# Kernel tuning notes

Hardware: AMD Instinct MI355X
Metric: run time of the kernel (lower is better)

Reference implementation:

```python
import jax, jax.numpy as jnp
import numpy as np

CHUNK_LEN = 32
N_HEAD = 32
HEAD_SIZE = 64
EPS = 1e-5 * 64.0  # GroupNorm eps = 1e-5 * head_size_divisor**2
PREC_MIN = 0.005   # rwkv_inner precision_min_val clamp for fp32


def rwkv_inner(r, k, v, w, u, kv_state, chunk_len):
    # r,k,v,w: [B,H,L,K]; u: [H,K]; kv_state: [B,H,K,V]
    B, H, L, K = k.shape
    T = chunk_len
    N = L // T
    w = jnp.clip(w, PREC_MIN, None)
    wc_log = jnp.log(w).reshape(B, H, N, T, K)
    wc_cum = jnp.cumsum(wc_log, axis=-2)                      # [B,H,N,T,K]
    shifted = jnp.concatenate([jnp.zeros_like(wc_cum[..., :1, :]), wc_cum[..., :-1, :]], axis=-2)
    ws_log = jnp.sum(wc_log, axis=-2, keepdims=True)          # [B,H,N,1,K]
    w_inter = jnp.exp(ws_log - wc_cum)                        # decay to end of chunk
    w_intra = jnp.exp(wc_cum - wc_log)                        # decay from start of chunk
    rc = r.reshape(B, H, N, T, K)
    kc = k.reshape(B, H, N, T, K)
    vc = v.reshape(B, H, N, T, K)
    # intra-chunk attention, log-space offset at T//2 for numerical stability
    off = shifted[..., T // 2:T // 2 + 1, :]
    r_decay = jnp.exp(shifted - off)
    k_inv_decay = jnp.exp(off - wc_cum)
    a = jnp.einsum('bhntk,bhnsk->bhnts', rc * r_decay, kc * k_inv_decay)
    a = jnp.tril(a, -1)
    diag = jnp.einsum('bhntk,bhntk->bhnt', rc, u[None, :, None, None, :] * kc)
    out = jnp.einsum('bhnts,bhnsv->bhntv', a, vc) + diag[..., None] * vc
    # per-chunk (k*w_inter)^T @ v contributions, then sequential state carry
    wkv = jnp.einsum('bhntk,bhntv->bhnkv', kc * w_inter, vc)  # [B,H,N,K,V]
    ws = jnp.exp(ws_log)[:, :, :, 0, :]                       # [B,H,N,K]

    def step(state, xs):
        ws_i, wkv_i = xs
        new_state = state * ws_i[..., None] + wkv_i
        return new_state, state

    final_state, states = jax.lax.scan(step, kv_state, (jnp.moveaxis(ws, 2, 0), jnp.moveaxis(wkv, 2, 0)))
    states = jnp.moveaxis(states, 0, 2)                       # [B,H,N,K,V]
    out = out + jnp.einsum('bhntk,bhnkv->bhntv', rc * w_intra, states)
    return out.reshape(B, H, L, K), final_state


def _forward(x, shift_state, wkv_state,
             time_maa_x, time_maa_w, time_maa_k, time_maa_v, time_maa_r, time_maa_g,
             time_maa_w1, time_maa_w2, time_decay, time_decay_w1, time_decay_w2,
             time_faaaa, Wr, Wk, Wv, Wg, Wo, gn_w, gn_b):
    B, T, C = x.shape
    H, K = N_HEAD, HEAD_SIZE
    xprev = jnp.concatenate([shift_state[:, None, :], x[:, :-1]], axis=1)
    dx = xprev - x
    # token-shift LoRA mixing
    xxx = jnp.tanh((x + dx * time_maa_x) @ time_maa_w1).reshape(B, T, 5, -1)
    m = jnp.einsum('btfe,fec->fbtc', xxx, time_maa_w2)  # [5,B,T,C]
    mw, mk, mv, mr, mg = m[0], m[1], m[2], m[3], m[4]
    xk = x + dx * (time_maa_k + mk)
    xv = x + dx * (time_maa_v + mv)
    xr = x + dx * (time_maa_r + mr)
    xg = x + dx * (time_maa_g + mg)
    xw = x + dx * (time_maa_w + mw)
    r = (xr @ Wr.T).reshape(B, T, H, K).transpose(0, 2, 1, 3)
    k = (xk @ Wk.T).reshape(B, T, H, K).transpose(0, 2, 1, 3)
    v = (xv @ Wv.T).reshape(B, T, H, K).transpose(0, 2, 1, 3)
    g = jax.nn.silu(xg @ Wg.T)
    w = time_decay.reshape(1, H, 1, K) + (jnp.tanh(xw @ time_decay_w1) @ time_decay_w2).reshape(B, T, H, K).transpose(0, 2, 1, 3)
    w = jnp.exp(-jnp.exp(w))
    out, wkv_out = rwkv_inner(r, k, v, w, time_faaaa, wkv_state, CHUNK_LEN)
    out = out.transpose(0, 2, 1, 3).reshape(B, T, C)
    # GroupNorm with H groups of K channels
    og = out.reshape(B, T, H, K)
    mu = og.mean(-1, keepdims=True)
    var = og.var(-1, keepdims=True)
    og = (og - mu) * jax.lax.rsqrt(var + EPS)
    out = og.reshape(B, T, C) * gn_w + gn_b
    out = (out * g) @ Wo.T
    return out, x[:, -1], wkv_out


def setup_inputs() -> dict:
    B, T, C = 4, 2048, 2048
    H, K = N_HEAD, HEAD_SIZE
    E5, TD = 32, 64
    key = jax.random.key(0)
    ks = jax.random.split(key, 24)
    f32 = jnp.float32
    inp = {
        'x': jax.random.normal(ks[0], (B, T, C), f32),
        'shift_state': jax.random.normal(ks[1], (B, C), f32),
        'wkv_state': jax.random.normal(ks[2], (B, H, K, K), f32) * 0.1,
        'time_maa_x': jax.random.uniform(ks[3], (1, 1, C), f32),
        'time_maa_w': jax.random.uniform(ks[4], (1, 1, C), f32),
        'time_maa_k': jax.random.uniform(ks[5], (1, 1, C), f32),
        'time_maa_v': jax.random.uniform(ks[6], (1, 1, C), f32),
        'time_maa_r': jax.random.uniform(ks[7], (1, 1, C), f32),
        'time_maa_g': jax.random.uniform(ks[8], (1, 1, C), f32),
        'time_maa_w1': jax.random.uniform(ks[9], (C, E5 * 5), f32, -1e-4, 1e-4),
        'time_maa_w2': jax.random.normal(ks[10], (5, E5, C), f32) * 0.01,
        'time_decay': jnp.linspace(-6.0, -1.0, C, dtype=f32).reshape(1, 1, C),
        'time_decay_w1': jax.random.uniform(ks[11], (C, TD), f32, -1e-4, 1e-4),
        'time_decay_w2': jax.random.normal(ks[12], (TD, C), f32) * 0.01,
        'time_faaaa': jax.random.normal(ks[13], (H, K), f32) * 0.1,
        'Wr': jax.random.normal(ks[14], (C, C), f32) * 0.02,
        'Wk': jax.random.normal(ks[15], (C, C), f32) * 0.02,
        'Wv': jax.random.normal(ks[16], (C, C), f32) * 0.02,
        'Wg': jax.random.normal(ks[17], (C, C), f32) * 0.02,
        'Wo': jax.random.normal(ks[18], (C, C), f32) * 0.02,
        'gn_w': jnp.ones((C,), f32),
        'gn_b': jnp.zeros((C,), f32),
    }
    return inp


def reference(x, shift_state, wkv_state,
              time_maa_x, time_maa_w, time_maa_k, time_maa_v, time_maa_r, time_maa_g,
              time_maa_w1, time_maa_w2, time_decay, time_decay_w1, time_decay_w2,
              time_faaaa, Wr, Wk, Wv, Wg, Wo, gn_w, gn_b):
    return _forward(x, shift_state, wkv_state,
                    time_maa_x, time_maa_w, time_maa_k, time_maa_v, time_maa_r, time_maa_g,
                    time_maa_w1, time_maa_w2, time_decay, time_decay_w1, time_decay_w2,
                    time_faaaa, Wr, Wk, Wv, Wg, Wo, gn_w, gn_b)
```

## Files before the change

### kernel.cpp

```cpp
#include <hip/hip_runtime.h>
#include <stdint.h>
#include <math.h>


typedef __attribute__((ext_vector_type(8))) short bf16x8;
typedef __attribute__((ext_vector_type(4))) float f32x4;

#define AS1(p) ((const __attribute__((address_space(1))) void*)(p))
#define AS3(p) ((__attribute__((address_space(3))) void*)(p))

__device__ __forceinline__ unsigned short f2bf(float f) {
  unsigned int u = __builtin_bit_cast(unsigned int, f);
  u += 0x7fffu + ((u >> 16) & 1u);
  return (unsigned short)(u >> 16);
}
__device__ __forceinline__ float bf2f(unsigned short s) {
  unsigned int u = ((unsigned int)s) << 16;
  return __builtin_bit_cast(float, u);
}

template <int EPI, bool BOUNDS>
__global__ __launch_bounds__(256) void gemm_nt(
    const unsigned short* __restrict__ A, const unsigned short* __restrict__ B,
    void* __restrict__ Cp, int M, int N, int K, const float* __restrict__ evec,
    int slot)
{
  __shared__ __align__(16) unsigned short As[128 * 32];
  __shared__ __align__(16) unsigned short Bs[128 * 32];
  const int tid = threadIdx.x;
  const int l = tid & 63, w = tid >> 6;
  const int wm = w & 1, wn = w >> 1;
  const int lm = l & 15, quad = l >> 4;
  const long mBase = (long)blockIdx.y * 128;
  const long nBase = (long)blockIdx.x * 128;

  f32x4 acc[4][4];
  f32x4 zero = {0.f, 0.f, 0.f, 0.f};
#pragma unroll
  for (int i = 0; i < 4; i++)
#pragma unroll
    for (int j = 0; j < 4; j++) acc[i][j] = zero;

  for (int k0 = 0; k0 < K; k0 += 32) {
    if (!BOUNDS) {
      const int r0 = w * 32;
      const int lr = l >> 2, lc = l & 3;
      const unsigned short* gA = A + (mBase + r0 + lr) * (long)K + k0 + lc * 8;
      __builtin_amdgcn_global_load_lds(AS1(gA), AS3(&As[r0 * 32]), 16, 0, 0);
      const unsigned short* gA2 = gA + 16 * (long)K;
      __builtin_amdgcn_global_load_lds(AS1(gA2), AS3(&As[(r0 + 16) * 32]), 16, 0, 0);
      const unsigned short* gB = B + (nBase + r0 + lr) * (long)K + k0 + lc * 8;
      __builtin_amdgcn_global_load_lds(AS1(gB), AS3(&Bs[r0 * 32]), 16, 0, 0);
      const unsigned short* gB2 = gB + 16 * (long)K;
      __builtin_amdgcn_global_load_lds(AS1(gB2), AS3(&Bs[(r0 + 16) * 32]), 16, 0, 0);
    } else {
      const int row = tid >> 2, ch = tid & 3;
#pragma unroll
      for (int rr = 0; rr < 128; rr += 64) {
        int r = rr + row;
        *(int4*)&As[r * 32 + ch * 8] =
            *(const int4*)&A[(mBase + r) * (long)K + k0 + ch * 8];
        int4 bv = make_int4(0, 0, 0, 0);
        long nG = nBase + r;
        if (nG < N) bv = *(const int4*)&B[nG * (long)K + k0 + ch * 8];
        *(int4*)&Bs[r * 32 + ch * 8] = bv;
      }
    }
    __syncthreads();
    bf16x8 af[4], bq[4];
#pragma unroll
    for (int i = 0; i < 4; i++)
      af[i] = *(const bf16x8*)&As[(wm * 64 + i * 16 + lm) * 32 + quad * 8];
#pragma unroll
    for (int i = 0; i < 4; i++)
      bq[i] = *(const bf16x8*)&Bs[(wn * 64 + i * 16 + lm) * 32 + quad * 8];
#pragma unroll
    for (int mi = 0; mi < 4; mi++)
#pragma unroll
      for (int ni = 0; ni < 4; ni++)
        acc[mi][ni] = __builtin_amdgcn_mfma_f32_16x16x32_bf16(af[mi], bq[ni], acc[mi][ni], 0, 0, 0);
    __syncthreads();
  }

#pragma unroll
  for (int mi = 0; mi < 4; mi++) {
#pragma unroll
    for (int ni = 0; ni < 4; ni++) {
      long col = nBase + wn * 64 + ni * 16 + lm;
      if (BOUNDS && col >= N) continue;
      long rw0 = mBase + wm * 64 + mi * 16 + quad * 4;
#pragma unroll
      for (int r = 0; r < 4; r++) {
        float y = acc[mi][ni][r];
        long row = rw0 + r;
        long off = row * (long)N + col;
        if constexpr (EPI == 0) {
          ((float*)Cp)[off] = y;
        } else if constexpr (EPI == 2) {
          ((unsigned short*)Cp)[off] = f2bf(tanhf(y));
        } else if constexpr (EPI == 3) {
          ((unsigned short*)Cp)[off] = f2bf(y / (1.f + __expf(-y)));
        } else if constexpr (EPI == 4) {
          float wv = evec[col] + y;
          ((_Float16*)Cp)[off] = (_Float16)fmaxf(-__expf(wv), -5.2983174f);
        } else if constexpr (EPI == 5) {
          int b = (int)(row >> 11), t = (int)(row & 2047);
          int n = t >> 5, tt = t & 31;
          int h = (int)(col >> 6), kk = (int)(col & 63);
          long c = ((long)(b * 32 + h)) * 64 + n;
          ((unsigned short*)Cp)[c * 6144 + slot + tt * 64 + kk] = f2bf(y);
        }
      }
    }
  }
}

template <int EPI>
__global__ __launch_bounds__(512, 1) void gemm256_nt(
    const unsigned short* __restrict__ A, const unsigned short* __restrict__ B,
    void* __restrict__ Cp, int M, int N, int K, int slot)
{
  __shared__ __align__(16) unsigned short As2[2][16384];
  __shared__ __align__(16) unsigned short Bs2[2][16384];
  const int tid = threadIdx.x;
  const int l = tid & 63;
  const int w = tid >> 6;
  const int wm = w >> 2, wn = w & 3;
  const int lm = l & 15, quad = l >> 4;
  const long mBase = (long)blockIdx.y * 256;
  const long nBase = (long)blockIdx.x * 256;
  const int NT = K >> 6;

  const int r0 = tid >> 3;
  const int csw = (tid & 7) ^ (r0 & 7);
  const int ldsOff = (tid & ~63) * 8;
  const unsigned short* ga0 = A + (mBase + r0) * (long)K + csw * 8;
  const unsigned short* gb0 = B + (nBase + r0) * (long)K + csw * 8;

  f32x4 acc[8][4];
  f32x4 zero = {0.f, 0.f, 0.f, 0.f};
#pragma unroll
  for (int i = 0; i < 8; i++)
#pragma unroll
    for (int j = 0; j < 4; j++) acc[i][j] = zero;

#define STAGE256(kt_)                                                          \
  {                                                                            \
    const int _b = (kt_) & 1;                                                  \
    const unsigned short* _ga = ga0 + (long)(kt_) * 64;                        \
    const unsigned short* _gb = gb0 + (long)(kt_) * 64;                        \
    __builtin_amdgcn_global_load_lds(AS1(_ga), AS3(&As2[_b][ldsOff]), 16, 0, 0);              \
    __builtin_amdgcn_global_load_lds(AS1(_gb), AS3(&Bs2[_b][ldsOff]), 16, 0, 0);              \
    __builtin_amdgcn_global_load_lds(AS1(_ga + (long)64 * K), AS3(&As2[_b][4096 + ldsOff]), 16, 0, 0);  \
    __builtin_amdgcn_global_load_lds(AS1(_gb + (long)64 * K), AS3(&Bs2[_b][4096 + ldsOff]), 16, 0, 0);  \
    __builtin_amdgcn_global_load_lds(AS1(_ga + (long)128 * K), AS3(&As2[_b][8192 + ldsOff]), 16, 0, 0); \
    __builtin_amdgcn_global_load_lds(AS1(_gb + (long)128 * K), AS3(&Bs2[_b][8192 + ldsOff]), 16, 0, 0); \
    __builtin_amdgcn_global_load_lds(AS1(_ga + (long)192 * K), AS3(&As2[_b][12288 + ldsOff]), 16, 0, 0);\
    __builtin_amdgcn_global_load_lds(AS1(_gb + (long)192 * K), AS3(&Bs2[_b][12288 + ldsOff]), 16, 0, 0);\
  }

  STAGE256(0);
  STAGE256(1);
  asm volatile("s_waitcnt vmcnt(8)" ::: "memory");
  __builtin_amdgcn_s_barrier();

  const int q0 = (quad ^ (lm & 7)) * 8;
  const int rA = (wm * 128 + lm) * 64;
  const int rB = (wn * 64 + lm) * 64;

  for (int kt = 0; kt < NT; ++kt) {
    const int b = kt & 1;
    bf16x8 af[8][2], bq[4][2];
#pragma unroll
    for (int fm = 0; fm < 8; fm++)
      af[fm][0] = *(const bf16x8*)&As2[b][rA + fm * 1024 + q0];
#pragma unroll
    for (int fn = 0; fn < 4; fn++)
      bq[fn][0] = *(const bf16x8*)&Bs2[b][rB + fn * 1024 + q0];
#pragma unroll
    for (int fm = 0; fm < 8; fm++)
      af[fm][1] = *(const bf16x8*)&As2[b][rA + fm * 1024 + (q0 ^ 32)];
#pragma unroll
    for (int fn = 0; fn < 4; fn++)
      bq[fn][1] = *(const bf16x8*)&Bs2[b][rB + fn * 1024 + (q0 ^ 32)];

    __builtin_amdgcn_s_setprio(1);
#pragma unroll
    for (int fm = 0; fm < 8; fm++)
#pragma unroll
      for (int fn = 0; fn < 4; fn++)
        acc[fm][fn] = __builtin_amdgcn_mfma_f32_16x16x32_bf16(af[fm][0], bq[fn][0], acc[fm][fn], 0, 0, 0);
    __builtin_amdgcn_s_setprio(0);

    asm volatile("s_waitcnt lgkmcnt(0)" ::: "memory");
    __builtin_amdgcn_s_barrier();
    if (kt + 2 < NT) STAGE256(kt + 2);

    __builtin_amdgcn_s_setprio(1);
#pragma unroll
    for (int fm = 0; fm < 8; fm++)
#pragma unroll
      for (int fn = 0; fn < 4; fn++)
        acc[fm][fn] = __builtin_amdgcn_mfma_f32_16x16x32_bf16(af[fm][1], bq[fn][1], acc[fm][fn], 0, 0, 0);
    __builtin_amdgcn_s_setprio(0);

    if (kt + 2 < NT) {
      asm volatile("s_waitcnt vmcnt(8)" ::: "memory");
    } else {
      asm volatile("s_waitcnt vmcnt(0)" ::: "memory");
    }
    __builtin_amdgcn_s_barrier();
  }
#undef STAGE256

#pragma unroll
  for (int mi = 0; mi < 8; mi++) {
#pragma unroll
    for (int ni = 0; ni < 4; ni++) {
      long col = nBase + wn * 64 + ni * 16 + lm;
      long rw0 = mBase + wm * 128 + mi * 16 + quad * 4;
#pragma unroll
      for (int r = 0; r < 4; r++) {
        float y = acc[mi][ni][r];
        long row = rw0 + r;
        long off = row * (long)N + col;
        if constexpr (EPI == 0) {
          ((float*)Cp)[off] = y;
        } else if constexpr (EPI == 3) {
          ((unsigned short*)Cp)[off] = f2bf(y / (1.f + __expf(-y)));
        } else if constexpr (EPI == 5) {
          int bb = (int)(row >> 11), t = (int)(row & 2047);
          int n = t >> 5, tt = t & 31;
          int h = (int)(col >> 6), kk = (int)(col & 63);
          long c = ((long)(bb * 32 + h)) * 64 + n;
          ((unsigned short*)Cp)[c * 6144 + slot + tt * 64 + kk] = f2bf(y);
        }
      }
    }
  }
}

__global__ __launch_bounds__(256) void k_convert(const float* __restrict__ s,
                                                 unsigned short* __restrict__ d, int n4)
{
  int i = blockIdx.x * 256 + threadIdx.x;
  if (i >= n4) return;
  float4 v = ((const float4*)s)[i];
  short4 o;
  o.x = (short)f2bf(v.x); o.y = (short)f2bf(v.y);
  o.z = (short)f2bf(v.z); o.w = (short)f2bf(v.w);
  ((short4*)d)[i] = o;
}

__global__ __launch_bounds__(256) void k_transpose(const float* __restrict__ s,
                                                   unsigned short* __restrict__ d, int R, int C)
{
  int i = blockIdx.x * 256 + threadIdx.x;
  if (i >= R * C) return;
  int r = i / C, c = i - r * C;
  d[(long)c * R + r] = f2bf(s[i]);
}

__global__ __launch_bounds__(256) void k_prep(const float* __restrict__ x,
                                              const float* __restrict__ shift,
                                              const float* __restrict__ maax,
                                              unsigned short* __restrict__ xmix,
                                              float* __restrict__ xlast)
{
  int i = blockIdx.x * 256 + threadIdx.x;
  int c4 = (i & 511) * 4;
  long bt = i >> 9;
  int t = (int)(bt & 2047);
  long b = bt >> 11;
  float4 xv = *(const float4*)&x[bt * 2048 + c4];
  float4 xp;
  if (t == 0) xp = *(const float4*)&shift[b * 2048 + c4];
  else        xp = *(const float4*)&x[(bt - 1) * 2048 + c4];
  float4 mx = *(const float4*)&maax[c4];
  short4 o;
  o.x = (short)f2bf(xv.x + (xp.x - xv.x) * mx.x);
  o.y = (short)f2bf(xv.y + (xp.y - xv.y) * mx.y);
  o.z = (short)f2bf(xv.z + (xp.z - xv.z) * mx.z);
  o.w = (short)f2bf(xv.w + (xp.w - xv.w) * mx.w);
  *(short4*)&xmix[bt * 2048 + c4] = o;
  if (t == 2047) *(float4*)&xlast[b * 2048 + c4] = xv;
}

__global__ __launch_bounds__(256) void k_mix1(
    const unsigned short* __restrict__ xxx, const unsigned short* __restrict__ w2t,
    const float* __restrict__ x, const float* __restrict__ shift,
    const float* __restrict__ maa, unsigned short* __restrict__ xout, int f)
{
  __shared__ __align__(16) unsigned short As[128 * 32];
  __shared__ __align__(16) unsigned short Bs[128 * 32];
  const int tid = threadIdx.x;
  const int l = tid & 63, w = tid >> 6;
  const int wm = w & 1, wn = w >> 1;
  const int lm = l & 15, quad = l >> 4;
  const long mBase = (long)blockIdx.y * 128;
  const long nBase = (long)blockIdx.x * 128;
  const int row = tid >> 2, ch = tid & 3;
#pragma unroll
  for (int rr = 0; rr < 128; rr += 64) {
    int r = rr + row;
    *(int4*)&As[r * 32 + ch * 8] =
        *(const int4*)&xxx[(mBase + r) * 160 + f * 32 + ch * 8];
    *(int4*)&Bs[r * 32 + ch * 8] =
        *(const int4*)&w2t[((long)f * 2048 + nBase + r) * 32 + ch * 8];
  }
  __syncthreads();
  f32x4 zero = {0.f, 0.f, 0.f, 0.f};
  f32x4 acc[4][4];
#pragma unroll
  for (int i = 0; i < 4; i++)
#pragma unroll
    for (int j = 0; j < 4; j++) acc[i][j] = zero;
  bf16x8 af[4], bq[4];
#pragma unroll
  for (int i = 0; i < 4; i++)
    af[i] = *(const bf16x8*)&As[(wm * 64 + i * 16 + lm) * 32 + quad * 8];
#pragma unroll
  for (int i = 0; i < 4; i++)
    bq[i] = *(const bf16x8*)&Bs[(wn * 64 + i * 16 + lm) * 32 + quad * 8];
#pragma unroll
  for (int mi = 0; mi < 4; mi++)
#pragma unroll
    for (int ni = 0; ni < 4; ni++)
      acc[mi][ni] = __builtin_amdgcn_mfma_f32_16x16x32_bf16(af[mi], bq[ni], acc[mi][ni], 0, 0, 0);

#pragma unroll
  for (int mi = 0; mi < 4; mi++) {
#pragma unroll
    for (int ni = 0; ni < 4; ni++) {
      long col = nBase + wn * 64 + ni * 16 + lm;
#pragma unroll
      for (int r = 0; r < 4; r++) {
        long rg = mBase + wm * 64 + mi * 16 + quad * 4 + r;
        int t = (int)(rg & 2047);
        long b = rg >> 11;
        float xval = x[rg * 2048 + col];
        float xp = t ? x[(rg - 1) * 2048 + col] : shift[b * 2048 + col];
        float res = xval + (xp - xval) * (maa[col] + acc[mi][ni][r]);
        xout[rg * 2048 + col] = f2bf(res);
      }
    }
  }
}

__global__ __launch_bounds__(256) void k_chunk(
    unsigned short* __restrict__ recs, const _Float16* __restrict__ wl,
    const float* __restrict__ u, float* __restrict__ outw,
    float* __restrict__ wsb)
{
  const int chunk = blockIdx.x;
  const int n = chunk & 63, bh = chunk >> 6;
  const int h = bh & 31, b = bh >> 5;
  const int tid = threadIdx.x;
  const int lane = tid & 63, wvid = tid >> 6;
  const long rec = (long)chunk * 6144;
  const long tbase = ((long)(b * 2048 + n * 32)) * 2048 + h * 64;

  __shared__ float vc[32][65];
  __shared__ float wcum[32][65];
  __shared__ float rdec[32][65];
  __shared__ float kdec[32][65];
  __shared__ float amat[32][33];
  __shared__ float wsk[64];

  float rcr[8], kcr[8];
#pragma unroll
  for (int j = 0; j < 8; j++) {
    int t = wvid + 4 * j;
    long g = rec + t * 64 + lane;
    rcr[j] = bf2f(recs[g]);
    kcr[j] = bf2f(recs[g + 2048]);
    vc[t][lane] = bf2f(recs[g + 4096]);
    wcum[t][lane] = (float)wl[tbase + (long)t * 2048 + lane];
  }
  float uval = u[h * 64 + lane];
  __syncthreads();

  if (tid < 64) {
    float run = 0.f;
    for (int t = 0; t < 32; t++) { run += wcum[t][tid]; wcum[t][tid] = run; }
    wsk[tid] = run;
  }
  __syncthreads();

  const float offv = wcum[15][lane];
  const float wsv = wsk[lane];
  float rdr[8], kdr[8], klr[8], rwir[8], dpart[8];
#pragma unroll
  for (int j = 0; j < 8; j++) {
    int t = wvid + 4 * j;
    float cw = wcum[t][lane];
    float sh = t ? wcum[t - 1][lane] : 0.f;
    rwir[j] = rcr[j] * __expf(sh);
    rdr[j] = rcr[j] * __expf(sh - offv);
    kdr[j] = kcr[j] * __expf(offv - cw);
    klr[j] = kcr[j] * __expf(wsv - cw);
    dpart[j] = rcr[j] * uval * kcr[j];
  }
  __syncthreads();

#pragma unroll
  for (int j = 0; j < 8; j++) {
    int t = wvid + 4 * j;
    rdec[t][lane] = rdr[j];
    kdec[t][lane] = kdr[j];
    wcum[t][lane] = klr[j];
    recs[rec + 4096 + t * 64 + lane] = f2bf(rwir[j]);
  }
  if (tid < 64) wsb[(long)chunk * 64 + tid] = __expf(wsk[tid]);
  __syncthreads();

  {
    const int t0 = (tid >> 4) * 2, s0 = (tid & 15) * 2;
    float a00 = 0, a01 = 0, a10 = 0, a11 = 0;
    for (int kk = 0; kk < 64; kk++) {
      float r0 = rdec[t0][kk], r1 = rdec[t0 + 1][kk];
      float c0 = kdec[s0][kk], c1 = kdec[s0 + 1][kk];
      a00 += r0 * c0; a01 += r0 * c1; a10 += r1 * c0; a11 += r1 * c1;
    }
    amat[t0][s0]         = (s0     < t0)     ? a00 : 0.f;
    amat[t0][s0 + 1]     = (s0 + 1 < t0)     ? a01 : 0.f;
    amat[t0 + 1][s0]     = (s0     < t0 + 1) ? a10 : 0.f;
    amat[t0 + 1][s0 + 1] = (s0 + 1 < t0 + 1) ? a11 : 0.f;
  }
  __syncthreads();
#pragma unroll
  for (int j = 0; j < 8; j++) {
    float d = dpart[j];
#pragma unroll
    for (int m = 32; m; m >>= 1) d += __shfl_xor(d, m, 64);
    if (lane == 0) amat[wvid + 4 * j][wvid + 4 * j] = d;
  }
  __syncthreads();

  {
    const int t0 = (tid >> 4) * 2, v0 = (tid & 15) * 4;
    float o00 = 0, o01 = 0, o02 = 0, o03 = 0, o10 = 0, o11 = 0, o12 = 0, o13 = 0;
    for (int s = 0; s < 32; s++) {
      float a0 = amat[t0][s], a1 = amat[t0 + 1][s];
      float b0 = vc[s][v0], b1 = vc[s][v0 + 1], b2 = vc[s][v0 + 2], b3 = vc[s][v0 + 3];
      o00 += a0 * b0; o01 += a0 * b1; o02 += a0 * b2; o03 += a0 * b3;
      o10 += a1 * b0; o11 += a1 * b1; o12 += a1 * b2; o13 += a1 * b3;
    }
    float* p0 = &outw[tbase + (long)t0 * 2048 + v0];
    float* p1 = &outw[tbase + (long)(t0 + 1) * 2048 + v0];
    p0[0] = o00; p0[1] = o01; p0[2] = o02; p0[3] = o03;
    p1[0] = o10; p1[1] = o11; p1[2] = o12; p1[3] = o13;
  }

  {
    const int kk0 = (tid >> 4) * 4, v0 = (tid & 15) * 4;
    float a[4][4];
#pragma unroll
    for (int i = 0; i < 4; i++)
#pragma unroll
      for (int j = 0; j < 4; j++) a[i][j] = 0.f;
    for (int t = 0; t < 32; t++) {
      float w0 = wcum[t][kk0], w1 = wcum[t][kk0 + 1], w2 = wcum[t][kk0 + 2], w3 = wcum[t][kk0 + 3];
      float b0 = vc[t][v0], b1 = vc[t][v0 + 1], b2 = vc[t][v0 + 2], b3 = vc[t][v0 + 3];
      a[0][0] += w0 * b0; a[0][1] += w0 * b1; a[0][2] += w0 * b2; a[0][3] += w0 * b3;
      a[1][0] += w1 * b0; a[1][1] += w1 * b1; a[1][2] += w1 * b2; a[1][3] += w1 * b3;
      a[2][0] += w2 * b0; a[2][1] += w2 * b1; a[2][2] += w2 * b2; a[2][3] += w2 * b3;
      a[3][0] += w3 * b0; a[3][1] += w3 * b1; a[3][2] += w3 * b2; a[3][3] += w3 * b3;
    }
#pragma unroll
    for (int i = 0; i < 4; i++)
#pragma unroll
      for (int j = 0; j < 4; j++)
        recs[rec + (kk0 + i) * 64 + v0 + j] = f2bf(a[i][j]);
  }
}

__global__ __launch_bounds__(256) void k_scan(unsigned short* __restrict__ recs,
                                              const float* __restrict__ wsb,
                                              const float* __restrict__ kv0,
                                              float* __restrict__ finalst)
{
  const int bh = blockIdx.x >> 2;
  const int kq = blockIdx.x & 3;
  const int tid = threadIdx.x;
  float st[4];
  const long base = (long)bh * 4096 + kq * 1024;
#pragma unroll
  for (int j = 0; j < 4; j++) st[j] = kv0[base + j * 256 + tid];
  for (int n = 0; n < 64; n++) {
    const long cb = ((long)bh * 64 + n) * 6144 + kq * 1024;
    const long wb = ((long)bh * 64 + n) * 64 + kq * 16;
#pragma unroll
    for (int j = 0; j < 4; j++) {
      int i = j * 256 + tid;
      unsigned short* p = &recs[cb + i];
      float wv = bf2f(*p);
      *p = f2bf(st[j]);
      st[j] = st[j] * wsb[wb + (i >> 6)] + wv;
    }
  }
#pragma unroll
  for (int j = 0; j < 4; j++) finalst[base + j * 256 + tid] = st[j];
}

__global__ __launch_bounds__(256) void k_inter(const unsigned short* __restrict__ recs,
                                               float* __restrict__ outw)
{
  const int chunk = blockIdx.x;
  const int n = chunk & 63, bh = chunk >> 6;
  const int h = bh & 31, b = bh >> 5;
  const int tid = threadIdx.x;
  __shared__ float st[64][65];
  __shared__ float rw[32][65];
  const long rec = (long)chunk * 6144;
  for (int i = tid; i < 4096; i += 256) st[i >> 6][i & 63] = bf2f(recs[rec + i]);
  for (int i = tid; i < 2048; i += 256) rw[i >> 6][i & 63] = bf2f(recs[rec + 4096 + i]);
  __syncthreads();
  const long tbase = ((long)(b * 2048 + n * 32)) * 2048 + h * 64;
  const int t0 = (tid >> 4) * 2, v0 = (tid & 15) * 4;
  float o00 = 0, o01 = 0, o02 = 0, o03 = 0, o10 = 0, o11 = 0, o12 = 0, o13 = 0;
  for (int kk = 0; kk < 64; kk++) {
    float r0 = rw[t0][kk], r1 = rw[t0 + 1][kk];
    float s0 = st[kk][v0], s1 = st[kk][v0 + 1], s2 = st[kk][v0 + 2], s3 = st[kk][v0 + 3];
    o00 += r0 * s0; o01 += r0 * s1; o02 += r0 * s2; o03 += r0 * s3;
    o10 += r1 * s0; o11 += r1 * s1; o12 += r1 * s2; o13 += r1 * s3;
  }
  float* p0 = &outw[tbase + (long)t0 * 2048 + v0];
  float* p1 = &outw[tbase + (long)(t0 + 1) * 2048 + v0];
  p0[0] += o00; p0[1] += o01; p0[2] += o02; p0[3] += o03;
  p1[0] += o10; p1[1] += o11; p1[2] += o12; p1[3] += o13;
}

__global__ __launch_bounds__(256) void k_gnorm(const float* __restrict__ outw,
                                               const unsigned short* __restrict__ gb,
                                               const float* __restrict__ gnw,
                                               const float* __restrict__ gnb,
                                               unsigned short* __restrict__ aout)
{
  const int gid = blockIdx.x * 4 + (threadIdx.x >> 6);
  const int lane = threadIdx.x & 63;
  const long bt = gid >> 5;
  const int h = gid & 31;
  const int c = h * 64 + lane;
  const long off = bt * 2048 + c;
  float y = outw[off];
  float s = y, sq = y * y;
#pragma unroll
  for (int m = 32; m; m >>= 1) {
    s += __shfl_xor(s, m, 64);
    sq += __shfl_xor(sq, m, 64);
  }
  float mu = s * (1.f / 64.f);
  float var = sq * (1.f / 64.f) - mu * mu;
  float nrm = (y - mu) * rsqrtf(var + 6.4e-4f);
  float o = (nrm * gnw[c] + gnb[c]) * bf2f(gb[off]);
  aout[off] = f2bf(o);
}

extern "C" void kernel_launch(void* const* d_in, const int* in_sizes, int n_in,
                              void* d_out, int out_size, void* d_ws, size_t ws_size,
                              hipStream_t stream)
{
  const float* x     = (const float*)d_in[0];
  const float* shift = (const float*)d_in[1];
  const float* kv0   = (const float*)d_in[2];
  const float* maax  = (const float*)d_in[3];
  const float* maaw  = (const float*)d_in[4];
  const float* maak  = (const float*)d_in[5];
  const float* maav  = (const float*)d_in[6];
  const float* maar  = (const float*)d_in[7];
  const float* maag  = (const float*)d_in[8];
  const float* w1    = (const float*)d_in[9];
  const float* w2    = (const float*)d_in[10];
  const float* tdec  = (const float*)d_in[11];
  const float* tdw1  = (const float*)d_in[12];
  const float* tdw2  = (const float*)d_in[13];
  const float* u     = (const float*)d_in[14];
  const float* Wr    = (const float*)d_in[15];
  const float* Wk    = (const float*)d_in[16];
  const float* Wv    = (const float*)d_in[17];
  const float* Wg    = (const float*)d_in[18];
  const float* Wo    = (const float*)d_in[19];
  const float* gnw   = (const float*)d_in[20];
  const float* gnb   = (const float*)d_in[21];

  char* ws = (char*)d_ws;
  const size_t MB = 1048576;
  unsigned short* WbfR  = (unsigned short*)(ws + 0 * MB);
  unsigned short* WbfK  = (unsigned short*)(ws + 8 * MB);
  unsigned short* WbfV  = (unsigned short*)(ws + 16 * MB);
  unsigned short* WbfG  = (unsigned short*)(ws + 24 * MB);
  unsigned short* WbfO  = (unsigned short*)(ws + 32 * MB);
  unsigned short* w2tb  = (unsigned short*)(ws + 40 * MB);
  unsigned short* w1t   = (unsigned short*)(ws + 40 * MB + 655360);
  unsigned short* tdw1t = (unsigned short*)(ws + 40 * MB + 1310720);
  unsigned short* tdw2t = (unsigned short*)(ws + 40 * MB + 1572864);
  unsigned short* xxxb  = (unsigned short*)(ws + 40 * MB + 1835008);
  unsigned short* t1b   = (unsigned short*)(ws + 40 * MB + 4456448);
  float*          wsb   = (float*)(ws + 40 * MB + 5505024);
  unsigned short* xmixb = (unsigned short*)(ws + 48 * MB);
  _Float16*       wlb   = (_Float16*)(ws + 48 * MB);
  unsigned short* x1b   = (unsigned short*)(ws + 80 * MB);
  unsigned short* aob   = (unsigned short*)(ws + 80 * MB);
  unsigned short* recs  = (unsigned short*)(ws + 112 * MB);
  unsigned short* gbuf  = recs;

  float* outp    = (float*)d_out;
  float* xlast   = outp + 16777216;
  float* finalst = outp + 16777216 + 8192;

  k_convert<<<4096, 256, 0, stream>>>(Wr, WbfR, 1048576);
  k_convert<<<4096, 256, 0, stream>>>(Wk, WbfK, 1048576);
  k_convert<<<4096, 256, 0, stream>>>(Wv, WbfV, 1048576);
  k_convert<<<4096, 256, 0, stream>>>(Wg, WbfG, 1048576);
  k_convert<<<4096, 256, 0, stream>>>(Wo, WbfO, 1048576);
  k_transpose<<<1280, 256, 0, stream>>>(w1, w1t, 2048, 160);
  k_transpose<<<512, 256, 0, stream>>>(tdw1, tdw1t, 2048, 64);
  k_transpose<<<512, 256, 0, stream>>>(tdw2, tdw2t, 64, 2048);
  for (int f = 0; f < 5; f++)
    k_transpose<<<256, 256, 0, stream>>>(w2 + (long)f * 65536, w2tb + (long)f * 65536, 32, 2048);

  k_prep<<<16384, 256, 0, stream>>>(x, shift, maax, xmixb, xlast);
  gemm_nt<2, true><<<dim3(2, 64), 256, 0, stream>>>(xmixb, w1t, xxxb, 8192, 160, 2048, nullptr, 0);

  k_mix1<<<dim3(16, 64), 256, 0, stream>>>(xxxb, w2tb, x, shift, maaw, x1b, 0);
  gemm_nt<2, true><<<dim3(1, 64), 256, 0, stream>>>(x1b, tdw1t, t1b, 8192, 64, 2048, nullptr, 0);
  gemm_nt<4, false><<<dim3(16, 64), 256, 0, stream>>>(t1b, tdw2t, wlb, 8192, 2048, 64, tdec, 0);
  k_mix1<<<dim3(16, 64), 256, 0, stream>>>(xxxb, w2tb, x, shift, maak, x1b, 1);
  gemm256_nt<5><<<dim3(8, 32), 512, 0, stream>>>(x1b, WbfK, recs, 8192, 2048, 2048, 2048);
  k_mix1<<<dim3(16, 64), 256, 0, stream>>>(xxxb, w2tb, x, shift, maav, x1b, 2);
  gemm256_nt<5><<<dim3(8, 32), 512, 0, stream>>>(x1b, WbfV, recs, 8192, 2048, 2048, 4096);
  k_mix1<<<dim3(16, 64), 256, 0, stream>>>(xxxb, w2tb, x, shift, maar, x1b, 3);
  gemm256_nt<5><<<dim3(8, 32), 512, 0, stream>>>(x1b, WbfR, recs, 8192, 2048, 2048, 0);
  k_mix1<<<dim3(16, 64), 256, 0, stream>>>(xxxb, w2tb, x, shift, maag, x1b, 4);

  k_chunk<<<8192, 256, 0, stream>>>(recs, wlb, u, outp, wsb);
  k_scan<<<512, 256, 0, stream>>>(recs, wsb, kv0, finalst);
  k_inter<<<8192, 256, 0, stream>>>(recs, outp);

  gemm256_nt<3><<<dim3(8, 32), 512, 0, stream>>>(x1b, WbfG, gbuf, 8192, 2048, 2048, 0);
  k_gnorm<<<65536, 256, 0, stream>>>(outp, gbuf, gnw, gnb, aob);
  gemm256_nt<0><<<dim3(8, 32), 512, 0, stream>>>(aob, WbfO, outp, 8192, 2048, 2048, 0);
}
```

Baseline: 1.281 ms.

## Use bf16 MFMA with hi/lo split in chunk and inter-chunk kernels

Replaces scalar FP32 shared-memory matmuls in k_chunk (A·V and k_decay^T·V) and k_inter (r·state) with 16x16x32 bf16 MFMA instructions. Values are staged transposed in shared memory, and the attention matrix and decayed keys are split into hi/lo bf16 pairs to keep close to fp32 accuracy. The per-chunk cumulative-sum is also parallelised across waves using partial sums instead of a single 64-thread serial loop. The chunk and inter kernels are a small share of the total runtime, which is likely dominated by the large GEMMs. The extra split MFMAs and transposed stores cost some work in exchange.

```diff
diff --git a/kernel.cpp b/kernel.cpp
--- a/kernel.cpp
+++ b/kernel.cpp
@@ -17,6 +17,9 @@
 __device__ __forceinline__ float bf2f(unsigned short s) {
   unsigned int u = ((unsigned int)s) << 16;
   return __builtin_bit_cast(float, u);
+}
+__device__ __forceinline__ unsigned int packbf(float lo, float hi) {
+  return (unsigned int)f2bf(lo) | ((unsigned int)f2bf(hi) << 16);
 }
 
 template <int EPI, bool BOUNDS>
@@ -356,122 +359,157 @@
   const int n = chunk & 63, bh = chunk >> 6;
   const int h = bh & 31, b = bh >> 5;
   const int tid = threadIdx.x;
-  const int lane = tid & 63, wvid = tid >> 6;
+  const int lane = tid & 63, w = tid >> 6;
+  const int lm = lane & 15, quad = lane >> 4;
   const long rec = (long)chunk * 6144;
   const long tbase = ((long)(b * 2048 + n * 32)) * 2048 + h * 64;
 
-  __shared__ float vc[32][65];
-  __shared__ float wcum[32][65];
-  __shared__ float rdec[32][65];
-  __shared__ float kdec[32][65];
-  __shared__ float amat[32][33];
-  __shared__ float wsk[64];
-
-  float rcr[8], kcr[8];
+  __shared__ float rdec[32][68];
+  __shared__ float kdec[32][68];
+  __shared__ float ssum[4][64];
+  __shared__ float offr[64];
+  __shared__ float diagr[32];
+  __shared__ __align__(16) unsigned short amatH[32][40];
+  __shared__ __align__(16) unsigned short amatL[32][40];
+  __shared__ __align__(16) unsigned short vcT[64][40];
+  __shared__ __align__(16) unsigned short kwH[64][40];
+  __shared__ __align__(16) unsigned short kwL[64][40];
+
+  float rv[8], kv[8], wlog[8], cum[8];
 #pragma unroll
   for (int j = 0; j < 8; j++) {
-    int t = wvid + 4 * j;
+    int t = w * 8 + j;
     long g = rec + t * 64 + lane;
-    rcr[j] = bf2f(recs[g]);
-    kcr[j] = bf2f(recs[g + 2048]);
-    vc[t][lane] = bf2f(recs[g + 4096]);
-    wcum[t][lane] = (float)wl[tbase + (long)t * 2048 + lane];
-  }
-  float uval = u[h * 64 + lane];
+    rv[j] = bf2f(recs[g]);
+    kv[j] = bf2f(recs[g + 2048]);
+    wlog[j] = (float)wl[tbase + (long)t * 2048 + lane];
+  }
+  {
+    float run = 0.f;
+#pragma unroll
+    for (int j = 0; j < 8; j++) { run += wlog[j]; cum[j] = run; }
+    ssum[w][lane] = run;
+  }
+#pragma unroll
+  for (int jp = 0; jp < 4; jp++) {
+    int t0 = w * 8 + jp * 2;
+    float v0 = bf2f(recs[rec + (t0) * 64 + lane + 4096]);
+    float v1 = bf2f(recs[rec + (t0 + 1) * 64 + lane + 4096]);
+    *(unsigned int*)&vcT[lane][t0] = packbf(v0, v1);
+  }
   __syncthreads();
 
-  if (tid < 64) {
-    float run = 0.f;
-    for (int t = 0; t < 32; t++) { run += wcum[t][tid]; wcum[t][tid] = run; }
-    wsk[tid] = run;
-  }
+  float off = 0.f, tot = 0.f;
+#pragma unroll
+  for (int w2 = 0; w2 < 4; w2++) {
+    float s2 = ssum[w2][lane];
+    tot += s2;
+    if (w2 < w) off += s2;
+  }
+#pragma unroll
+  for (int j = 0; j < 8; j++) cum[j] += off;
+  if (w == 1) offr[lane] = cum[7];
+  if (w == 0) wsb[(long)chunk * 64 + lane] = __expf(tot);
   __syncthreads();
 
-  const float offv = wcum[15][lane];
-  const float wsv = wsk[lane];
-  float rdr[8], kdr[8], klr[8], rwir[8], dpart[8];
+  const float offv = offr[lane];
+  const float uval = u[h * 64 + lane];
+#pragma unroll
+  for (int jp = 0; jp < 4; jp++) {
+    unsigned short h2[2], l2[2];
+#pragma unroll
+    for (int p = 0; p < 2; p++) {
+      int j = jp * 2 + p;
+      int t = w * 8 + j;
+      float cw = cum[j];
+      float sh = cw - wlog[j];
+      rdec[t][lane] = rv[j] * __expf(sh - offv);
+      kdec[t][lane] = kv[j] * __expf(offv - cw);
+      float kw_ = kv[j] * __expf(tot - cw);
+      h2[p] = f2bf(kw_);
+      l2[p] = f2bf(kw_ - bf2f(h2[p]));
+      recs[rec + 4096 + t * 64 + lane] = f2bf(rv[j] * __expf(sh));
+    }
+    *(unsigned int*)&kwH[lane][w * 8 + jp * 2] = (unsigned int)h2[0] | ((unsigned int)h2[1] << 16);
+    *(unsigned int*)&kwL[lane][w * 8 + jp * 2] = (unsigned int)l2[0] | ((unsigned int)l2[1] << 16);
+  }
 #pragma unroll
   for (int j = 0; j < 8; j++) {
-    int t = wvid + 4 * j;
-    float cw = wcum[t][lane];
-    float sh = t ? wcum[t - 1][lane] : 0.f;
-    rwir[j] = rcr[j] * __expf(sh);
-    rdr[j] = rcr[j] * __expf(sh - offv);
-    kdr[j] = kcr[j] * __expf(offv - cw);
-    klr[j] = kcr[j] * __expf(wsv - cw);
-    dpart[j] = rcr[j] * uval * kcr[j];
+    float d = rv[j] * uval * kv[j];
+#pragma unroll
+    for (int m = 32; m; m >>= 1) d += __shfl_xor(d, m, 64);
+    if (lane == 0) diagr[w * 8 + j] = d;
   }
   __syncthreads();
 
-#pragma unroll
-  for (int j = 0; j < 8; j++) {
-    int t = wvid + 4 * j;
-    rdec[t][lane] = rdr[j];
-    kdec[t][lane] = kdr[j];
-    wcum[t][lane] = klr[j];
-    recs[rec + 4096 + t * 64 + lane] = f2bf(rwir[j]);
-  }
-  if (tid < 64) wsb[(long)chunk * 64 + tid] = __expf(wsk[tid]);
+  {
+    const int t0 = (tid >> 4) * 2;
+    const int sA = tid & 15;
+    float a00 = 0, a01 = 0, a10 = 0, a11 = 0;
+#pragma unroll
+    for (int kk = 0; kk < 64; kk += 4) {
+      float4 r0 = *(const float4*)&rdec[t0][kk];
+      float4 r1 = *(const float4*)&rdec[t0 + 1][kk];
+      float4 c0 = *(const float4*)&kdec[sA][kk];
+      float4 c1 = *(const float4*)&kdec[sA + 16][kk];
+      a00 += r0.x * c0.x + r0.y * c0.y + r0.z * c0.z + r0.w * c0.w;
+      a01 += r0.x * c1.x + r0.y * c1.y + r0.z * c1.z + r0.w * c1.w;
+      a10 += r1.x * c0.x + r1.y * c0.y + r1.z * c0.z + r1.w * c0.w;
+      a11 += r1.x * c1.x + r1.y * c1.y + r1.z * c1.z + r1.w * c1.w;
+    }
+    const int sB = sA + 16;
+    float m00 = sA < t0 ? a00 : (sA == t0 ? diagr[t0] : 0.f);
+    float m01 = sB < t0 ? a01 : (sB == t0 ? diagr[t0] : 0.f);
+    float m10 = sA < t0 + 1 ? a10 : (sA == t0 + 1 ? diagr[t0 + 1] : 0.f);
+    float m11 = sB < t0 + 1 ? a11 : (sB == t0 + 1 ? diagr[t0 + 1] : 0.f);
+    unsigned short h00 = f2bf(m00), h01 = f2bf(m01), h10 = f2bf(m10), h11 = f2bf(m11);
+    amatH[t0][sA] = h00;     amatL[t0][sA] = f2bf(m00 - bf2f(h00));
+    amatH[t0][sB] = h01;     amatL[t0][sB] = f2bf(m01 - bf2f(h01));
+    amatH[t0 + 1][sA] = h10; amatL[t0 + 1][sA] = f2bf(m10 - bf2f(h10));
+    amatH[t0 + 1][sB] = h11; amatL[t0 + 1][sB] = f2bf(m11 - bf2f(h11));
+  }
   __syncthreads();
 
   {
-    const int t0 = (tid >> 4) * 2, s0 = (tid & 15) * 2;
-    float a00 = 0, a01 = 0, a10 = 0, a11 = 0;
-    for (int kk = 0; kk < 64; kk++) {
-      float r0 = rdec[t0][kk], r1 = rdec[t0 + 1][kk];
-      float c0 = kdec[s0][kk], c1 = kdec[s0 + 1][kk];
-      a00 += r0 * c0; a01 += r0 * c1; a10 += r1 * c0; a11 += r1 * c1;
-    }
-    amat[t0][s0]         = (s0     < t0)     ? a00 : 0.f;
-    amat[t0][s0 + 1]     = (s0 + 1 < t0)     ? a01 : 0.f;
-    amat[t0 + 1][s0]     = (s0     < t0 + 1) ? a10 : 0.f;
-    amat[t0 + 1][s0 + 1] = (s0 + 1 < t0 + 1) ? a11 : 0.f;
-  }
-  __syncthreads();
-#pragma unroll
-  for (int j = 0; j < 8; j++) {
-    float d = dpart[j];
-#pragma unroll
-    for (int m = 32; m; m >>= 1) d += __shfl_xor(d, m, 64);
-    if (lane == 0) amat[wvid + 4 * j][wvid + 4 * j] = d;
-  }
-  __syncthreads();
-
-  {
-    const int t0 = (tid >> 4) * 2, v0 = (tid & 15) * 4;
-    float o00 = 0, o01 = 0, o02 = 0, o03 = 0, o10 = 0, o11 = 0, o12 = 0, o13 = 0;
-    for (int s = 0; s < 32; s++) {
-      float a0 = amat[t0][s], a1 = amat[t0 + 1][s];
-      float b0 = vc[s][v0], b1 = vc[s][v0 + 1], b2 = vc[s][v0 + 2], b3 = vc[s][v0 + 3];
-      o00 += a0 * b0; o01 += a0 * b1; o02 += a0 * b2; o03 += a0 * b3;
-      o10 += a1 * b0; o11 += a1 * b1; o12 += a1 * b2; o13 += a1 * b3;
-    }
-    float* p0 = &outw[tbase + (long)t0 * 2048 + v0];
-    float* p1 = &outw[tbase + (long)(t0 + 1) * 2048 + v0];
-    p0[0] = o00; p0[1] = o01; p0[2] = o02; p0[3] = o03;
-    p1[0] = o10; p1[1] = o11; p1[2] = o12; p1[3] = o13;
-  }
-
-  {
-    const int kk0 = (tid >> 4) * 4, v0 = (tid & 15) * 4;
-    float a[4][4];
-#pragma unroll
-    for (int i = 0; i < 4; i++)
-#pragma unroll
-      for (int j = 0; j < 4; j++) a[i][j] = 0.f;
-    for (int t = 0; t < 32; t++) {
-      float w0 = wcum[t][kk0], w1 = wcum[t][kk0 + 1], w2 = wcum[t][kk0 + 2], w3 = wcum[t][kk0 + 3];
-      float b0 = vc[t][v0], b1 = vc[t][v0 + 1], b2 = vc[t][v0 + 2], b3 = vc[t][v0 + 3];
-      a[0][0] += w0 * b0; a[0][1] += w0 * b1; a[0][2] += w0 * b2; a[0][3] += w0 * b3;
-      a[1][0] += w1 * b0; a[1][1] += w1 * b1; a[1][2] += w1 * b2; a[1][3] += w1 * b3;
-      a[2][0] += w2 * b0; a[2][1] += w2 * b1; a[2][2] += w2 * b2; a[2][3] += w2 * b3;
-      a[3][0] += w3 * b0; a[3][1] += w3 * b1; a[3][2] += w3 * b2; a[3][3] += w3 * b3;
-    }
-#pragma unroll
-    for (int i = 0; i < 4; i++)
-#pragma unroll
-      for (int j = 0; j < 4; j++)
-        recs[rec + (kk0 + i) * 64 + v0 + j] = f2bf(a[i][j]);
+    bf16x8 bv[4];
+#pragma unroll
+    for (int ni = 0; ni < 4; ni++)
+      bv[ni] = *(const bf16x8*)&vcT[ni * 16 + lm][quad * 8];
+
+    const int ti = w >> 1;
+    bf16x8 avh = *(const bf16x8*)&amatH[ti * 16 + lm][quad * 8];
+    bf16x8 avl = *(const bf16x8*)&amatL[ti * 16 + lm][quad * 8];
+    bf16x8 akh = *(const bf16x8*)&kwH[w * 16 + lm][quad * 8];
+    bf16x8 akl = *(const bf16x8*)&kwL[w * 16 + lm][quad * 8];
+
+    f32x4 zero = {0.f, 0.f, 0.f, 0.f};
+    f32x4 oc0 = zero, oc1 = zero;
+    const int nA = (w & 1) * 2;
+    oc0 = __builtin_amdgcn_mfma_f32_16x16x32_bf16(avh, bv[nA], oc0, 0, 0, 0);
+    oc0 = __builtin_amdgcn_mfma_f32_16x16x32_bf16(avl, bv[nA], oc0, 0, 0, 0);
+    oc1 = __builtin_amdgcn_mfma_f32_16x16x32_bf16(avh, bv[nA + 1], oc1, 0, 0, 0);
+    oc1 = __builtin_amdgcn_mfma_f32_16x16x32_bf16(avl, bv[nA + 1], oc1, 0, 0, 0);
+    f32x4 kc[4];
+#pragma unroll
+    for (int ni = 0; ni < 4; ni++) {
+      kc[ni] = zero;
+      kc[ni] = __builtin_amdgcn_mfma_f32_16x16x32_bf16(akh, bv[ni], kc[ni], 0, 0, 0);
+      kc[ni] = __builtin_amdgcn_mfma_f32_16x16x32_bf16(akl, bv[ni], kc[ni], 0, 0, 0);
+    }
+
+#pragma unroll
+    for (int r = 0; r < 4; r++) {
+      int t = ti * 16 + quad * 4 + r;
+      outw[tbase + (long)t * 2048 + nA * 16 + lm] = oc0[r];
+      outw[tbase + (long)t * 2048 + (nA + 1) * 16 + lm] = oc1[r];
+    }
+#pragma unroll
+    for (int ni = 0; ni < 4; ni++)
+#pragma unroll
+      for (int r = 0; r < 4; r++) {
+        int kk = w * 16 + quad * 4 + r;
+        recs[rec + kk * 64 + ni * 16 + lm] = f2bf(kc[ni][r]);
+      }
   }
 }
 
@@ -510,25 +548,47 @@
   const int n = chunk & 63, bh = chunk >> 6;
   const int h = bh & 31, b = bh >> 5;
   const int tid = threadIdx.x;
-  __shared__ float st[64][65];
-  __shared__ float rw[32][65];
+  const int lane = tid & 63, w = tid >> 6;
+  const int lm = lane & 15, quad = lane >> 4;
   const long rec = (long)chunk * 6144;
-  for (int i = tid; i < 4096; i += 256) st[i >> 6][i & 63] = bf2f(recs[rec + i]);
-  for (int i = tid; i < 2048; i += 256) rw[i >> 6][i & 63] = bf2f(recs[rec + 4096 + i]);
+  const long tbase = ((long)(b * 2048 + n * 32)) * 2048 + h * 64;
+
+  __shared__ __align__(16) unsigned short stT[64][72];
+  __shared__ __align__(16) unsigned short rwb[32][72];
+
+  {
+    int4 rwv = *(const int4*)&recs[rec + 4096 + tid * 8];
+    *(int4*)&rwb[tid >> 3][(tid & 7) * 8] = rwv;
+  }
+  for (int ii = tid; ii < 4096; ii += 256)
+    stT[ii & 63][ii >> 6] = recs[rec + ii];
   __syncthreads();
-  const long tbase = ((long)(b * 2048 + n * 32)) * 2048 + h * 64;
-  const int t0 = (tid >> 4) * 2, v0 = (tid & 15) * 4;
-  float o00 = 0, o01 = 0, o02 = 0, o03 = 0, o10 = 0, o11 = 0, o12 = 0, o13 = 0;
-  for (int kk = 0; kk < 64; kk++) {
-    float r0 = rw[t0][kk], r1 = rw[t0 + 1][kk];
-    float s0 = st[kk][v0], s1 = st[kk][v0 + 1], s2 = st[kk][v0 + 2], s3 = st[kk][v0 + 3];
-    o00 += r0 * s0; o01 += r0 * s1; o02 += r0 * s2; o03 += r0 * s3;
-    o10 += r1 * s0; o11 += r1 * s1; o12 += r1 * s2; o13 += r1 * s3;
-  }
-  float* p0 = &outw[tbase + (long)t0 * 2048 + v0];
-  float* p1 = &outw[tbase + (long)(t0 + 1) * 2048 + v0];
-  p0[0] += o00; p0[1] += o01; p0[2] += o02; p0[3] += o03;
-  p1[0] += o10; p1[1] += o11; p1[2] += o12; p1[3] += o13;
+
+  const int mi = w >> 1, nset = w & 1;
+  bf16x8 aA[2], bB[2][2];
+#pragma unroll
+  for (int kk = 0; kk < 2; kk++) {
+    aA[kk] = *(const bf16x8*)&rwb[mi * 16 + lm][kk * 32 + quad * 8];
+#pragma unroll
+    for (int p = 0; p < 2; p++)
+      bB[p][kk] = *(const bf16x8*)&stT[(nset * 2 + p) * 16 + lm][kk * 32 + quad * 8];
+  }
+  f32x4 zero = {0.f, 0.f, 0.f, 0.f};
+  f32x4 oc[2] = {zero, zero};
+#pragma unroll
+  for (int kk = 0; kk < 2; kk++) {
+    oc[0] = __builtin_amdgcn_mfma_f32_16x16x32_bf16(aA[kk], bB[0][kk], oc[0], 0, 0, 0);
+    oc[1] = __builtin_amdgcn_mfma_f32_16x16x32_bf16(aA[kk], bB[1][kk], oc[1], 0, 0, 0);
+  }
+#pragma unroll
+  for (int p = 0; p < 2; p++) {
+    int v = (nset * 2 + p) * 16 + lm;
+#pragma unroll
+    for (int r = 0; r < 4; r++) {
+      int t = mi * 16 + quad * 4 + r;
+      outw[tbase + (long)t * 2048 + v] += oc[p][r];
+    }
+  }
 }
 
 __global__ __launch_bounds__(256) void k_gnorm(const float* __restrict__ outw,
```

Result: faster. 1.240 ms (-3.2%).
